# Performance work log

Hardware: AMD Instinct MI355X
Metric: run time of the kernel (lower is better)

Reference implementation:

```python
import jax, jax.numpy as jnp
import numpy as np


def _prelu(x, a):
    return jnp.where(x >= 0, x, a * x)


def setup_inputs() -> dict:
    key = jax.random.key(0)
    ks = jax.random.split(key, 10)
    B, N, h_dim, H_dim, g_dim, Kc, n = 64, 4096, 256, 1024, 512, 32, 2048
    hs = jax.random.normal(ks[0], (B, N, h_dim), dtype=jnp.float32)
    cs_o = jax.random.randint(ks[1], (B, N), 0, Kc, dtype=jnp.int32)

    def lin(k, fi, fo):
        return jax.random.normal(k, (fi, fo), dtype=jnp.float32) / np.sqrt(fi).astype(np.float32)

    a = jnp.full((1,), 0.25, dtype=jnp.float32)  # torch PReLU default
    return {
        "hs": hs,
        "W1": lin(ks[2], h_dim, H_dim), "b1": jnp.zeros((H_dim,), jnp.float32), "a1": a,
        "W2": lin(ks[3], H_dim, H_dim), "b2": jnp.zeros((H_dim,), jnp.float32), "a2": a,
        "W3": lin(ks[4], H_dim, H_dim), "b3": jnp.zeros((H_dim,), jnp.float32), "a3": a,
        "W4": lin(ks[5], H_dim, H_dim), "b4": jnp.zeros((H_dim,), jnp.float32), "a4": a,
        "W5": lin(ks[6], H_dim, H_dim), "b5": jnp.zeros((H_dim,), jnp.float32), "a5": a,
        "W6": lin(ks[7], H_dim, g_dim), "b6": jnp.zeros((g_dim,), jnp.float32),
        "cs_o": cs_o,
        "n": n,
    }


def reference(hs, W1, b1, a1, W2, b2, a2, W3, b3, a3, W4, b4, a4, W5, b5, a5, W6, b6, cs_o, n):
    B, N, h_dim = hs.shape
    cs = cs_o.at[:, n:].set(-1)                  # points >= n are unassigned
    K = int(jnp.max(cs)) + 1                      # static (concrete data)
    Ks = jnp.max(cs, axis=1)                      # [B] max cluster id per batch entry

    # per-cluster masked sums (vectorized segment-sum over all K at once)
    onehot = (cs[:, :, None] == jnp.arange(K)[None, None, :]).astype(hs.dtype)  # [B,N,K]
    Hk = jnp.einsum('bnk,bnh->bkh', onehot, hs)   # [B,K,h] sum of hs per cluster
    hn = hs[:, n, :]                              # [B,h] the point being assigned
    # H = [H_0..H_{K-1}, H_0+h_n..H_{K-1}+h_n, h_n]
    H = jnp.concatenate([Hk, Hk + hn[:, None, :], hn[:, None, :]], axis=1)  # [B,2K+1,h]

    mk = (jnp.sum(onehot, axis=1) > 0).astype(hs.dtype)  # [B,K] cluster non-empty
    gs_mask = jnp.concatenate([mk, mk, jnp.ones((B, 1), hs.dtype)], axis=1)[:, :, None]

    # 6-layer MLP g applied to all B*(2K+1) rows at once
    x = H.reshape(B * (2 * K + 1), h_dim)
    x = _prelu(x @ W1 + b1, a1)
    x = _prelu(x @ W2 + b2, a2)
    x = _prelu(x @ W3 + b3, a3)
    x = _prelu(x @ W4 + b4, a4)
    x = _prelu(x @ W5 + b5, a5)
    gs = (x @ W6 + b6).reshape(B, 2 * K + 1, -1) * gs_mask  # [B,2K+1,g]

    # G_k = sum_{j<K, j!=k} gs_j + gs_{k+K} ;  G_K = sum_{j<K} gs_j + gs_{2K}
    S = jnp.sum(gs[:, :K], axis=1)                                   # [B,g]
    G_head = (S[:, None, :] - gs[:, :K] + gs[:, K:2 * K]) * mk[:, :, None]
    G_last = S + gs[:, 2 * K]
    G = jnp.concatenate([G_head, G_last[:, None, :]], axis=1)        # [B,K+1,g]

    # per-batch correction: if Ks[b]==k (k<K-1), move G[b,-1] to slot k+1, zero last
    need = (Ks >= 0) & (Ks < K - 1)
    kidx = jnp.arange(K + 1)
    move = need[:, None] & (kidx[None, :] == (Ks + 1)[:, None])      # [B,K+1]
    G = jnp.where(move[:, :, None], G[:, K:K + 1, :], G)
    G = jnp.where((need[:, None] & (kidx[None, :] == K))[:, :, None], 0.0, G)
    G_mask = jnp.where(need[:, None] & (kidx[None, :] >= (Ks + 2)[:, None]),
                       0.0, jnp.ones((B, K + 1), hs.dtype))
    return (G, G_mask)
```

## Files before the change

kernel.cpp:

```cpp
#include <hip/hip_runtime.h>
#include <hip/hip_bf16.h>
#include <stdint.h>

using bf16x8 = __attribute__((ext_vector_type(8))) short;
using f32x4  = __attribute__((ext_vector_type(4))) float;

#define BATCH 64
#define NTOK  4096
#define HD    256
#define HDIM  1024
#define GD    512

__device__ __forceinline__ ushort f2bf(float f) {
  union { __hip_bfloat16 h; ushort u; } cv;
  cv.h = __float2bfloat16(f);
  return cv.u;
}

__device__ __forceinline__ void gload_lds16(const void* gsrc, void* ldst) {
  typedef const __attribute__((address_space(1))) uint32_t* gas_p;
  typedef __attribute__((address_space(3))) uint32_t* las_p;
  __builtin_amdgcn_global_load_lds((gas_p)(uintptr_t)gsrc, (las_p)(uintptr_t)ldst, 16, 0, 0);
}

struct WTArgs {
  const float* src[6];
  ushort* dst[6];
  int fi[6];
  int fo[6];
};

__global__ __launch_bounds__(256) void pre_kernel(WTArgs a,
                                                  const int* __restrict__ cs,
                                                  const int* __restrict__ nptr,
                                                  int* __restrict__ idx,
                                                  int* __restrict__ off,
                                                  int* __restrict__ cnt,
                                                  int* __restrict__ Ks,
                                                  int K) {
  __shared__ int csb[NTOK];
  __shared__ ushort hist[256 * 32];
  __shared__ int segsum[8][32];
  __shared__ int btot[32];
  __shared__ int bbase[32];
  __shared__ int red[4];
  __shared__ float tile[32][33];
  int t = threadIdx.x;
  if (blockIdx.x < BATCH) {
    int b = blockIdx.x;
    int n = *nptr;
    const int* csrow = cs + (size_t)b * NTOK;
    int mymax = -1;
    for (int i = t; i < n; i += 256) { int v = csrow[i]; csb[i] = v; mymax = max(mymax, v); }
#pragma unroll
    for (int k = 0; k < 32; ++k) hist[t * 32 + k] = 0;
    __syncthreads();
    int chunkN = (n + 255) >> 8;
    for (int c = 0; c < chunkN; ++c) {
      int i = c * 256 + t;
      if (i < n) hist[t * 32 + csb[i]]++;
    }
    __syncthreads();
    int kb = t & 31, sg = t >> 5;
    {
      int run = 0;
      int r0 = sg * 32;
      for (int r = r0; r < r0 + 32; ++r) run += hist[r * 32 + kb];
      segsum[sg][kb] = run;
    }
    __syncthreads();
    if (t < 32) {
      int acc0 = 0;
      for (int s = 0; s < 8; ++s) { int v = segsum[s][t]; segsum[s][t] = acc0; acc0 += v; }
      btot[t] = acc0;
    }
    __syncthreads();
    {
      int run = segsum[sg][kb];
      int r0 = sg * 32;
      for (int r = r0; r < r0 + 32; ++r) {
        int tmp = hist[r * 32 + kb];
        hist[r * 32 + kb] = (ushort)run;
        run += tmp;
      }
    }
    if (t == 0) {
      int base = 0;
      for (int k = 0; k < K; ++k) { bbase[k] = base; base += btot[k]; }
    }
    __syncthreads();
    if (t < K) { off[b * K + t] = bbase[t]; cnt[b * K + t] = btot[t]; }
    int* idxb = idx + (size_t)b * NTOK;
    for (int c = 0; c < chunkN; ++c) {
      int i = c * 256 + t;
      if (i < n) {
        int k = csb[i];
        int s = bbase[k] + (int)(hist[t * 32 + k]++);
        idxb[s] = i;
      }
    }
    for (int o2 = 32; o2; o2 >>= 1) mymax = max(mymax, __shfl_down(mymax, o2));
    if ((t & 63) == 0) red[t >> 6] = mymax;
    __syncthreads();
    if (t == 0) {
      int r = red[0];
      for (int i = 1; i < 4; ++i) r = max(r, red[i]);
      Ks[b] = r;
    }
  } else {
    int f = blockIdx.x - BATCH;
    int z = 0;
    while (true) {
      int nb = (a.fo[z] >> 5) * (a.fi[z] >> 5);
      if (f < nb) break;
      f -= nb; ++z;
    }
    int ncx = a.fo[z] >> 5;
    int cx = f % ncx, cy = f / ncx;
    int c0 = cx * 32, r0 = cy * 32;
    int fo = a.fo[z], fi = a.fi[z];
    const float* W = a.src[z];
    ushort* Wt = a.dst[z];
    int tx = t & 31, ty = t >> 5;
#pragma unroll
    for (int j = 0; j < 4; ++j)
      tile[ty + j * 8][tx] = W[(size_t)(r0 + ty + j * 8) * fo + (c0 + tx)];
    __syncthreads();
#pragma unroll
    for (int j = 0; j < 4; ++j)
      Wt[(size_t)(c0 + ty + j * 8) * fi + (r0 + tx)] = f2bf(tile[tx][ty + j * 8]);
  }
}

__global__ __launch_bounds__(256) void aggregate2_kernel(const float* __restrict__ hs,
                                                         const int* __restrict__ idx,
                                                         const int* __restrict__ off,
                                                         const int* __restrict__ cnt,
                                                         const int* __restrict__ nptr,
                                                         ushort* __restrict__ X,
                                                         int K, int M, int Mpad) {
  int b = blockIdx.x / K, k = blockIdx.x % K;
  int t = threadIdx.x;
  int g = t >> 6, l = t & 63;
  int n = *nptr;
  int c = cnt[b * K + k];
  int o = off[b * K + k];
  const float* hsb = hs + (size_t)b * NTOK * HD;
  const int* ids = idx + (size_t)b * NTOK + o;
  __shared__ int sid[256];
  __shared__ float part[4][HD];
  float a0x = 0.f, a0y = 0.f, a0z = 0.f, a0w = 0.f;
  float a1x = 0.f, a1y = 0.f, a1z = 0.f, a1w = 0.f;
  float a2x = 0.f, a2y = 0.f, a2z = 0.f, a2w = 0.f;
  float a3x = 0.f, a3y = 0.f, a3z = 0.f, a3w = 0.f;
  for (int j0 = 0; j0 < c; j0 += 256) {
    __syncthreads();
    if (j0 + t < c) sid[t] = ids[j0 + t];
    __syncthreads();
    int lim = min(256, c - j0);
    int j = g;
    for (; j + 12 < lim; j += 16) {
      float4 v0 = ((const float4*)&hsb[(size_t)sid[j] * HD])[l];
      float4 v1 = ((const float4*)&hsb[(size_t)sid[j + 4] * HD])[l];
      float4 v2 = ((const float4*)&hsb[(size_t)sid[j + 8] * HD])[l];
      float4 v3 = ((const float4*)&hsb[(size_t)sid[j + 12] * HD])[l];
      a0x += v0.x; a0y += v0.y; a0z += v0.z; a0w += v0.w;
      a1x += v1.x; a1y += v1.y; a1z += v1.z; a1w += v1.w;
      a2x += v2.x; a2y += v2.y; a2z += v2.z; a2w += v2.w;
      a3x += v3.x; a3y += v3.y; a3z += v3.z; a3w += v3.w;
    }
    for (; j < lim; j += 4) {
      float4 v = ((const float4*)&hsb[(size_t)sid[j] * HD])[l];
      a0x += v.x; a0y += v.y; a0z += v.z; a0w += v.w;
    }
  }
  part[g][l * 4 + 0] = (a0x + a1x) + (a2x + a3x);
  part[g][l * 4 + 1] = (a0y + a1y) + (a2y + a3y);
  part[g][l * 4 + 2] = (a0z + a1z) + (a2z + a3z);
  part[g][l * 4 + 3] = (a0w + a1w) + (a2w + a3w);
  __syncthreads();
  float sum = ((part[0][t] + part[1][t]) + (part[2][t] + part[3][t]));
  float hn = hsb[(size_t)n * HD + t];
  int R = 2 * K + 1;
  X[((size_t)b * R + k) * HD + t]     = f2bf(sum);
  X[((size_t)b * R + K + k) * HD + t] = f2bf(sum + hn);
  if (k == 0) {
    X[((size_t)b * R + 2 * K) * HD + t] = f2bf(hn);
    for (int r = M + b; r < Mpad; r += BATCH) X[(size_t)r * HD + t] = 0;
  }
}

template <int NN, bool LAST>
__global__ __launch_bounds__(256, 4) void gemm_kernel(const ushort* __restrict__ A,
                                                      const ushort* __restrict__ Bt,
                                                      const float* __restrict__ bias,
                                                      const float* __restrict__ aptr,
                                                      void* __restrict__ Cout,
                                                      int N, int Kd) {
  __shared__ ushort As[2][2][96 * 32];
  __shared__ ushort Bs[2][2][NN * 32 * 32];
  int tid = threadIdx.x;
  int lane = tid & 63, w = tid >> 6;
  int wr = w >> 1, wc = w & 1;
  int fr = lane & 15, fq = lane >> 4;

  int nwg = gridDim.x;
  int flat = blockIdx.x;
  int q8 = nwg >> 3, r8 = nwg & 7;
  int xcd = flat & 7, loc = flat >> 3;
  int swz = (xcd < r8 ? xcd * (q8 + 1) : r8 * (q8 + 1) + (xcd - r8) * q8) + loc;
  int NC = N / (NN * 32);
  int brow = swz / NC, bcol = swz % NC;

  size_t row0 = (size_t)brow * 96;
  size_t col0 = (size_t)bcol * (NN * 32);

  const ushort* Abase = A + row0 * (size_t)Kd;
  const ushort* Bbase = Bt + col0 * (size_t)Kd;

  f32x4 acc[3][NN] = {};

  int qA0 = w * 64 + lane;
  int qA1 = 256 + w * 64 + lane;
  int rA0 = qA0 >> 2, kA0 = (qA0 & 3) * 8;
  int rA1 = qA1 >> 2, kA1 = (qA1 & 3) * 8;
  int rB = qA0 >> 2, kB = (qA0 & 3) * 8;

  auto stage = [&](int buf, int k0) {
#pragma unroll
    for (int h = 0; h < 2; ++h) {
      int kh = k0 + h * 32;
      gload_lds16(Abase + (size_t)rA0 * Kd + kh + kA0, &As[buf][h][(w * 64) * 8]);
      if (w < 2)
        gload_lds16(Abase + (size_t)rA1 * Kd + kh + kA1, &As[buf][h][(256 + w * 64) * 8]);
      if (NN == 2) {
        gload_lds16(Bbase + (size_t)rB * Kd + kh + kB, &Bs[buf][h][(w * 64) * 8]);
      } else {
        if (w < 2)
          gload_lds16(Bbase + (size_t)rB * Kd + kh + kB, &Bs[buf][h][(w * 64) * 8]);
      }
    }
  };

  int nt = Kd >> 6;
  int cur = 0;
  stage(0, 0);
  __syncthreads();
  for (int t = 0; t < nt; ++t) {
    if (t + 1 < nt) stage(cur ^ 1, (t + 1) * 64);
    bf16x8 af[2][3], bfv[2][NN];
#pragma unroll
    for (int h = 0; h < 2; ++h) {
#pragma unroll
      for (int m = 0; m < 3; ++m)
        af[h][m] = *(const bf16x8*)&As[cur][h][(wr * 48 + m * 16 + fr) * 32 + fq * 8];
#pragma unroll
      for (int nn = 0; nn < NN; ++nn)
        bfv[h][nn] = *(const bf16x8*)&Bs[cur][h][(wc * (NN * 16) + nn * 16 + fr) * 32 + fq * 8];
    }
#pragma unroll
    for (int h = 0; h < 2; ++h)
#pragma unroll
      for (int m = 0; m < 3; ++m)
#pragma unroll
        for (int nn = 0; nn < NN; ++nn)
          acc[m][nn] = __builtin_amdgcn_mfma_f32_16x16x32_bf16(af[h][m], bfv[h][nn], acc[m][nn], 0, 0, 0);
    __syncthreads();
    cur ^= 1;
  }

  float alpha = 0.f;
  if (!LAST) alpha = aptr[0];
#pragma unroll
  for (int nn = 0; nn < NN; ++nn) {
    size_t col = col0 + wc * (NN * 16) + nn * 16 + fr;
    float bv = bias[col];
#pragma unroll
    for (int m = 0; m < 3; ++m) {
      size_t rbase = row0 + wr * 48 + m * 16 + fq * 4;
#pragma unroll
      for (int j = 0; j < 4; ++j) {
        float v = acc[m][nn][j] + bv;
        if (!LAST) {
          v = (v >= 0.f) ? v : alpha * v;
          ((ushort*)Cout)[(rbase + j) * N + col] = f2bf(v);
        } else {
          ((float*)Cout)[(rbase + j) * N + col] = v;
        }
      }
    }
  }
}

__global__ __launch_bounds__(256) void final_kernel(const float* __restrict__ gs,
                                                    const int* __restrict__ counts,
                                                    const int* __restrict__ Ks,
                                                    float* __restrict__ out,
                                                    int K) {
  int b = blockIdx.x >> 1, half = blockIdx.x & 1;
  int t = threadIdx.x;
  int col = half * 256 + t;
  __shared__ float mk[64];
  __shared__ int sks;
  if (t < K) mk[t] = (counts[b * K + t] > 0) ? 1.f : 0.f;
  if (t == 0) sks = Ks[b];
  __syncthreads();
  int ks = sks;
  bool need = (ks >= 0) && (ks < K - 1);
  const float* g = gs + (size_t)b * (2 * K + 1) * GD;
  float S0 = 0.f;
  for (int k = 0; k < K; ++k) S0 += g[(size_t)k * GD + col] * mk[k];
  float gl0 = S0 + g[(size_t)(2 * K) * GD + col];
  float* G  = out + (size_t)b * (K + 1) * GD;
  float* Gm = out + (size_t)BATCH * (K + 1) * GD + (size_t)b * (K + 1);
  for (int kk = 0; kk <= K; ++kk) {
    float v0;
    if (kk == K)                   v0 = need ? 0.f : gl0;
    else if (need && kk == ks + 1) v0 = gl0;
    else v0 = mk[kk] * (S0 - g[(size_t)kk * GD + col] + g[(size_t)(K + kk) * GD + col]);
    G[(size_t)kk * GD + col] = v0;
  }
  if (half == 0 && t <= K) Gm[t] = (need && t >= ks + 2) ? 0.f : 1.f;
}

extern "C" void kernel_launch(void* const* d_in, const int* in_sizes, int n_in,
                              void* d_out, int out_size, void* d_ws, size_t ws_size,
                              hipStream_t stream) {
  const float* hs = (const float*)d_in[0];
  const float* W[6]  = {(const float*)d_in[1], (const float*)d_in[4], (const float*)d_in[7],
                        (const float*)d_in[10], (const float*)d_in[13], (const float*)d_in[16]};
  const float* bb[6] = {(const float*)d_in[2], (const float*)d_in[5], (const float*)d_in[8],
                        (const float*)d_in[11], (const float*)d_in[14], (const float*)d_in[17]};
  const float* aa[5] = {(const float*)d_in[3], (const float*)d_in[6], (const float*)d_in[9],
                        (const float*)d_in[12], (const float*)d_in[15]};
  const int* cs   = (const int*)d_in[18];
  const int* nptr = (const int*)d_in[19];
  float* out = (float*)d_out;

  int K = out_size / (BATCH * (GD + 1)) - 1;
  int M = BATCH * (2 * K + 1);
  int Mpad = (M + 95) / 96 * 96;

  char* base = (char*)d_ws;
  size_t off_b = 0;
  auto alloc = [&](size_t bytes) {
    char* p = base + off_b;
    off_b = (off_b + bytes + 255) & ~(size_t)255;
    return p;
  };
  ushort* W1t  = (ushort*)alloc((size_t)HDIM * HD * 2);
  ushort* W2t  = (ushort*)alloc((size_t)HDIM * HDIM * 2);
  ushort* W3t  = (ushort*)alloc((size_t)HDIM * HDIM * 2);
  ushort* W4t  = (ushort*)alloc((size_t)HDIM * HDIM * 2);
  ushort* W5bt = (ushort*)alloc((size_t)HDIM * HDIM * 2);
  ushort* W6t  = (ushort*)alloc((size_t)GD * HDIM * 2);
  int* idx     = (int*)alloc((size_t)BATCH * NTOK * 4);
  int* offb    = (int*)alloc((size_t)BATCH * K * 4);
  int* cntb    = (int*)alloc((size_t)BATCH * K * 4);
  int* Ksb     = (int*)alloc(BATCH * 4);
  ushort* X    = (ushort*)alloc((size_t)Mpad * HD * 2);
  ushort* Y0   = (ushort*)alloc((size_t)Mpad * HDIM * 2);
  ushort* Y1   = (ushort*)alloc((size_t)Mpad * HDIM * 2);
  float*  gsb  = (float*)alloc((size_t)Mpad * GD * 4);
  (void)ws_size; (void)n_in; (void)in_sizes;

  WTArgs wa;
  wa.src[0] = W[0]; wa.dst[0] = W1t;  wa.fi[0] = HD;   wa.fo[0] = HDIM;
  wa.src[1] = W[1]; wa.dst[1] = W2t;  wa.fi[1] = HDIM; wa.fo[1] = HDIM;
  wa.src[2] = W[2]; wa.dst[2] = W3t;  wa.fi[2] = HDIM; wa.fo[2] = HDIM;
  wa.src[3] = W[3]; wa.dst[3] = W4t;  wa.fi[3] = HDIM; wa.fo[3] = HDIM;
  wa.src[4] = W[4]; wa.dst[4] = W5bt; wa.fi[4] = HDIM; wa.fo[4] = HDIM;
  wa.src[5] = W[5]; wa.dst[5] = W6t;  wa.fi[5] = HDIM; wa.fo[5] = GD;
  int nbw = 0;
  for (int z = 0; z < 6; ++z) nbw += (wa.fo[z] / 32) * (wa.fi[z] / 32);
  hipLaunchKernelGGL(pre_kernel, dim3(BATCH + nbw), dim3(256), 0, stream,
                     wa, cs, nptr, idx, offb, cntb, Ksb, K);

  hipLaunchKernelGGL(aggregate2_kernel, dim3(BATCH * K), dim3(256), 0, stream,
                     hs, idx, offb, cntb, nptr, X, K, M, Mpad);

  dim3 blk(256);
  int NR = Mpad / 96;
  hipLaunchKernelGGL((gemm_kernel<2, false>), dim3(NR * (HDIM / 64)), blk, 0, stream, X,   W1t,  bb[0], aa[0], (void*)Y0, HDIM, HD);
  hipLaunchKernelGGL((gemm_kernel<2, false>), dim3(NR * (HDIM / 64)), blk, 0, stream, Y0,  W2t,  bb[1], aa[1], (void*)Y1, HDIM, HDIM);
  hipLaunchKernelGGL((gemm_kernel<2, false>), dim3(NR * (HDIM / 64)), blk, 0, stream, Y1,  W3t,  bb[2], aa[2], (void*)Y0, HDIM, HDIM);
  hipLaunchKernelGGL((gemm_kernel<2, false>), dim3(NR * (HDIM / 64)), blk, 0, stream, Y0,  W4t,  bb[3], aa[3], (void*)Y1, HDIM, HDIM);
  hipLaunchKernelGGL((gemm_kernel<2, false>), dim3(NR * (HDIM / 64)), blk, 0, stream, Y1,  W5bt, bb[4], aa[4], (void*)Y0, HDIM, HDIM);
  hipLaunchKernelGGL((gemm_kernel<1, true>),  dim3(NR * (GD / 32)),   blk, 0, stream, Y0,  W6t,  bb[5], nullptr, (void*)gsb, GD, HDIM);

  hipLaunchKernelGGL(final_kernel, dim3(BATCH * 2), dim3(256), 0, stream, gsb, cntb, Ksb, out, K);
}
```

Baseline: 135.8 us.

## Deepen GEMM LDS pipeline to four stages with split loader warps

Replaces the double-buffered 64-wide K-step GEMM mainloop with a 4-slot ring of 32-wide K tiles, prefetching two tiles ahead. Loading is split so waves 0-1 fetch A and waves 2-3 fetch B. Explicit vmcnt waits plus a single s_barrier per step replace the trailing __syncthreads. The aim is more loads in flight and fewer full barriers so global-to-LDS latency overlaps MFMA work. The risks are an unbalanced load split, a correctness hazard in slot reuse (a slot is refilled two steps after use with only one barrier in between), and twice as many loop iterations.

```diff
diff --git a/kernel.cpp b/kernel.cpp
--- a/kernel.cpp
+++ b/kernel.cpp
@@ -197,8 +197,8 @@
                                                       const float* __restrict__ aptr,
                                                       void* __restrict__ Cout,
                                                       int N, int Kd) {
-  __shared__ ushort As[2][2][96 * 32];
-  __shared__ ushort Bs[2][2][NN * 32 * 32];
+  __shared__ ushort As[4][96 * 32];
+  __shared__ ushort Bs[4][NN * 32 * 32];
   int tid = threadIdx.x;
   int lane = tid & 63, w = tid >> 6;
   int wr = w >> 1, wc = w & 1;
@@ -220,54 +220,58 @@
 
   f32x4 acc[3][NN] = {};
 
-  int qA0 = w * 64 + lane;
-  int qA1 = 256 + w * 64 + lane;
-  int rA0 = qA0 >> 2, kA0 = (qA0 & 3) * 8;
-  int rA1 = qA1 >> 2, kA1 = (qA1 & 3) * 8;
-  int rB = qA0 >> 2, kB = (qA0 & 3) * 8;
-
   auto stage = [&](int buf, int k0) {
-#pragma unroll
-    for (int h = 0; h < 2; ++h) {
-      int kh = k0 + h * 32;
-      gload_lds16(Abase + (size_t)rA0 * Kd + kh + kA0, &As[buf][h][(w * 64) * 8]);
-      if (w < 2)
-        gload_lds16(Abase + (size_t)rA1 * Kd + kh + kA1, &As[buf][h][(256 + w * 64) * 8]);
-      if (NN == 2) {
-        gload_lds16(Bbase + (size_t)rB * Kd + kh + kB, &Bs[buf][h][(w * 64) * 8]);
-      } else {
-        if (w < 2)
-          gload_lds16(Bbase + (size_t)rB * Kd + kh + kB, &Bs[buf][h][(w * 64) * 8]);
+    if (w < 2) {
+      int q0 = w * 64 + lane;
+#pragma unroll
+      for (int i = 0; i < 3; ++i) {
+        int q = q0 + i * 128;
+        int r = q >> 2, kc = (q & 3) * 8;
+        gload_lds16(Abase + (size_t)r * Kd + k0 + kc, &As[buf][q * 8]);
+      }
+    } else {
+      int q0 = (w - 2) * 64 + lane;
+#pragma unroll
+      for (int i = 0; i < NN; ++i) {
+        int q = q0 + i * 128;
+        int r = q >> 2, kc = (q & 3) * 8;
+        gload_lds16(Bbase + (size_t)r * Kd + k0 + kc, &Bs[buf][q * 8]);
       }
     }
   };
 
-  int nt = Kd >> 6;
-  int cur = 0;
+  auto compute = [&](int cur) {
+    bf16x8 af[3], bfv[NN];
+#pragma unroll
+    for (int m = 0; m < 3; ++m)
+      af[m] = *(const bf16x8*)&As[cur][(wr * 48 + m * 16 + fr) * 32 + fq * 8];
+#pragma unroll
+    for (int nn = 0; nn < NN; ++nn)
+      bfv[nn] = *(const bf16x8*)&Bs[cur][(wc * (NN * 16) + nn * 16 + fr) * 32 + fq * 8];
+#pragma unroll
+    for (int m = 0; m < 3; ++m)
+#pragma unroll
+      for (int nn = 0; nn < NN; ++nn)
+        acc[m][nn] = __builtin_amdgcn_mfma_f32_16x16x32_bf16(af[m], bfv[nn], acc[m][nn], 0, 0, 0);
+  };
+
+  int nt = Kd >> 5;
   stage(0, 0);
-  __syncthreads();
-  for (int t = 0; t < nt; ++t) {
-    if (t + 1 < nt) stage(cur ^ 1, (t + 1) * 64);
-    bf16x8 af[2][3], bfv[2][NN];
-#pragma unroll
-    for (int h = 0; h < 2; ++h) {
-#pragma unroll
-      for (int m = 0; m < 3; ++m)
-        af[h][m] = *(const bf16x8*)&As[cur][h][(wr * 48 + m * 16 + fr) * 32 + fq * 8];
-#pragma unroll
-      for (int nn = 0; nn < NN; ++nn)
-        bfv[h][nn] = *(const bf16x8*)&Bs[cur][h][(wc * (NN * 16) + nn * 16 + fr) * 32 + fq * 8];
-    }
-#pragma unroll
-    for (int h = 0; h < 2; ++h)
-#pragma unroll
-      for (int m = 0; m < 3; ++m)
-#pragma unroll
-        for (int nn = 0; nn < NN; ++nn)
-          acc[m][nn] = __builtin_amdgcn_mfma_f32_16x16x32_bf16(af[h][m], bfv[h][nn], acc[m][nn], 0, 0, 0);
-    __syncthreads();
-    cur ^= 1;
-  }
+  stage(1, 32);
+  for (int t = 0; t < nt - 2; ++t) {
+    stage((t + 2) & 3, (t + 2) * 32);
+    if (w < 2) asm volatile("s_waitcnt vmcnt(6)" ::: "memory");
+    else       asm volatile("s_waitcnt vmcnt(%0)" :: "i"(2 * NN) : "memory");
+    __builtin_amdgcn_s_barrier();
+    compute(t & 3);
+  }
+  if (w < 2) asm volatile("s_waitcnt vmcnt(3)" ::: "memory");
+  else       asm volatile("s_waitcnt vmcnt(%0)" :: "i"(NN) : "memory");
+  __builtin_amdgcn_s_barrier();
+  compute((nt - 2) & 3);
+  asm volatile("s_waitcnt vmcnt(0)" ::: "memory");
+  __builtin_amdgcn_s_barrier();
+  compute((nt - 1) & 3);
 
   float alpha = 0.f;
   if (!LAST) alpha = aptr[0];
```

Result: slower. 149.0 us (+9.7%).
